# Performance work log

Hardware: AMD Instinct MI355X
Metric: run time of the kernel (lower is better)

The kernel has to match this reference:

```python
import jax, jax.numpy as jnp
import numpy as np

B, T, D = 2, 2048, 2048
H, HKV, DH = 16, 4, 128  # n_heads, n_kv_heads, d_head
EPS = 1e-6


def _rms_norm(t):
    # normalize over last dim, no learned weight (matches F.rms_norm default)
    return t * jax.lax.rsqrt(jnp.mean(t * t, axis=-1, keepdims=True) + EPS)


def _ortho_rope(t, cos, sin):
    # t: (b, h, t, d); unfold(-1,2,2) -> even/odd pairs
    x0 = t[..., 0::2]  # (b,h,t,d/2)
    x1 = t[..., 1::2]
    y0 = x0 * cos - x1 * sin
    y1 = x1 * cos + x0 * sin
    # NOTE: concatenated halves (NOT re-interleaved), faithful to source
    return jnp.concatenate((y0, y1), axis=-1)


def setup_inputs() -> dict:
    key = jax.random.key(0)
    ks = jax.random.split(key, 10)
    return {
        "x": jax.random.normal(ks[0], (B, T, D), jnp.float32),
        "pos_ids": jnp.broadcast_to(jnp.arange(T, dtype=jnp.int64), (B, T)),
        "cos": jax.random.normal(ks[1], (T, DH // 2), jnp.float32),
        "sin": jax.random.normal(ks[2], (T, DH // 2), jnp.float32),
        "v1": jax.random.normal(ks[3], (B, HKV, T, DH), jnp.float32),
        "Wq": jax.random.normal(ks[4], (H * DH, D), jnp.float32) * (D ** -0.5),
        "Wk": jax.random.normal(ks[5], (HKV * DH, D), jnp.float32) * (D ** -0.5),
        "Wv": jax.random.normal(ks[6], (HKV * DH, D), jnp.float32) * (D ** -0.5),
        "Wo": jax.random.normal(ks[7], (D, D), jnp.float32) * (D ** -0.5),
        "gate_w": jax.random.normal(ks[8], (H, H), jnp.float32) * 0.1,
        "v_lamb": jnp.float32(0.5),
    }


def reference(x, pos_ids, cos, sin, v1, Wq, Wk, Wv, Wo, gate_w, v_lamb):
    b, t, _ = x.shape
    # fused QKV projections (Linear, no bias: x @ W.T), split to heads
    q = (x @ Wq.T).reshape(b, t, H, DH).transpose(0, 2, 1, 3)    # (b,H,t,d)
    k = (x @ Wk.T).reshape(b, t, HKV, DH).transpose(0, 2, 1, 3)  # (b,Hkv,t,d)
    v = (x @ Wv.T).reshape(b, t, HKV, DH).transpose(0, 2, 1, 3)
    # value residual: lerp(v, v1, lamb) = v + lamb*(v1 - v)
    v = v + v_lamb * (v1 - v)
    # QK RMSNorm then ortho RoPE
    q = _ortho_rope(_rms_norm(q), cos, sin)
    k = _ortho_rope(_rms_norm(k), cos, sin)
    # kv_cache.upsert modeled as prefill: k,v unchanged, causal block mask
    g = H // HKV  # GQA group size
    k = jnp.repeat(k, g, axis=1)  # (b,H,t,d)
    vfull = jnp.repeat(v, g, axis=1)
    scale = DH ** -0.5
    scores = jnp.einsum('bhqd,bhkd->bhqk', q, k) * scale
    causal = jnp.tril(jnp.ones((t, t), dtype=bool))
    scores = jnp.where(causal, scores, jnp.finfo(scores.dtype).min)
    attn = jax.nn.softmax(scores, axis=-1)
    y = jnp.einsum('bhqk,bhkd->bhqd', attn, vfull)  # (b,H,t,d)
    # per-head sigmoid gate from first n_heads channels of x
    gates = jax.nn.sigmoid(x[..., :H] @ gate_w.T)   # (b,t,H)
    y = y * gates.transpose(0, 2, 1)[..., None]     # (b,H,t,1)
    y = y.transpose(0, 2, 1, 3).reshape(b, t, H * DH)
    out = y @ Wo.T
    return (out, v1)
```

## Files before the change

kernel.cpp:

```cpp
#include <hip/hip_runtime.h>

typedef __bf16 bf16;
typedef __attribute__((ext_vector_type(8))) __bf16 bf16x8;
typedef __attribute__((ext_vector_type(4))) __bf16 bf16x4;
typedef __attribute__((ext_vector_type(4))) float f32x4;
typedef __attribute__((ext_vector_type(4))) short short4v;

#define BB 2
#define TT 2048
#define DD 2048
#define HH 16
#define HKV 4
#define DHD 128
#define NQKV 3072

__device__ __forceinline__ void gl_lds16(const bf16* g, bf16* l) {
    __builtin_amdgcn_global_load_lds(
        (const __attribute__((address_space(1))) void*)g,
        (__attribute__((address_space(3))) void*)l, 16, 0, 0);
}

__global__ void cvt_fuse(const float* __restrict__ x, const float* __restrict__ Wq,
                         const float* __restrict__ Wk, const float* __restrict__ Wv,
                         const float* __restrict__ Wo, const float* __restrict__ gw,
                         bf16* __restrict__ xb, bf16* __restrict__ wqkvb,
                         bf16* __restrict__ wob, float* __restrict__ gates) {
    const int blk = blockIdx.x, tid = threadIdx.x;
    const float* src; bf16* dst; int i;
    const bool isx = blk < 4096;
    if (isx)              { src = x;  dst = xb;              i = blk * 256 + tid; }
    else if (blk < 6144)  { src = Wq; dst = wqkvb;           i = (blk - 4096) * 256 + tid; }
    else if (blk < 6656)  { src = Wk; dst = wqkvb + 4194304; i = (blk - 6144) * 256 + tid; }
    else if (blk < 7168)  { src = Wv; dst = wqkvb + 5242880; i = (blk - 6656) * 256 + tid; }
    else                  { src = Wo; dst = wob;             i = (blk - 7168) * 256 + tid; }
    float4 a = ((const float4*)src)[i * 2];
    float4 b = ((const float4*)src)[i * 2 + 1];
    bf16x8 v;
    v[0] = (bf16)a.x; v[1] = (bf16)a.y; v[2] = (bf16)a.z; v[3] = (bf16)a.w;
    v[4] = (bf16)b.x; v[5] = (bf16)b.y; v[6] = (bf16)b.z; v[7] = (bf16)b.w;
    *(bf16x8*)(dst + (size_t)i * 8) = v;

    if (isx) {
        __shared__ float xs16[16];
        __shared__ float gws[256];
        gws[tid] = gw[tid];
        if (tid < 2) {
            xs16[tid * 8 + 0] = a.x; xs16[tid * 8 + 1] = a.y;
            xs16[tid * 8 + 2] = a.z; xs16[tid * 8 + 3] = a.w;
            xs16[tid * 8 + 4] = b.x; xs16[tid * 8 + 5] = b.y;
            xs16[tid * 8 + 6] = b.z; xs16[tid * 8 + 7] = b.w;
        }
        __syncthreads();
        if (tid < 16) {
            float z = 0.f;
#pragma unroll
            for (int j = 0; j < 16; j++) z += xs16[j] * gws[tid * 16 + j];
            gates[blk * 16 + tid] = 1.f / (1.f + __expf(-z));
        }
    }
}

template <int MODE>
__global__ void gemm_bt(const bf16* __restrict__ A, const bf16* __restrict__ Bw,
                        int M, int N, int K,
                        float* __restrict__ Cout,
                        bf16* __restrict__ qb, bf16* __restrict__ kb,
                        bf16* __restrict__ vtb,
                        const float* __restrict__ v1,
                        const float* __restrict__ cosb,
                        const float* __restrict__ sinb,
                        const float* __restrict__ lamp) {
    constexpr int SMEM_ELE = (MODE == 1) ? 17920 : 16384;
    __shared__ bf16 smem[SMEM_ELE];
    bf16* As = smem;
    bf16* Bs = smem + 8192;
    const int tid = threadIdx.x;
    const int w = tid >> 6, lane = tid & 63;
    const int l15 = lane & 15, quad = lane >> 4;

    const int nwg = gridDim.x * gridDim.y;
    int wg = blockIdx.y * gridDim.x + blockIdx.x;
    int swz = (wg & 7) * (nwg >> 3) + (wg >> 3);
    const int bx = swz % gridDim.x, by = swz / gridDim.x;
    const int m0 = by * 128, n0 = bx * 128;
    const int wm = (w & 1) * 64, wn = (w >> 1) * 64;

    f32x4 acc[4][4] = {};
    const int lrow = lane >> 2;
    const int scol = ((lane & 3) ^ ((lane >> 3) & 3)) * 8;
    const int xs = (quad ^ ((l15 >> 1) & 3)) * 8;

    for (int k0 = 0; k0 < K; k0 += 64) {
#pragma unroll
        for (int i = 0; i < 4; i++) {
            int c = w * 4 + i;
            int kc2 = c >> 3, rc = c & 7;
            int row = rc * 16 + lrow;
            int kk = k0 + kc2 * 32 + scol;
            gl_lds16(A + (size_t)(m0 + row) * K + kk, As + c * 512);
            gl_lds16(Bw + (size_t)(n0 + row) * K + kk, Bs + c * 512);
        }
        __syncthreads();
#pragma unroll
        for (int kc2 = 0; kc2 < 2; kc2++) {
            bf16x8 af[4], bfr[4];
#pragma unroll
            for (int mi = 0; mi < 4; mi++)
                af[mi] = *(const bf16x8*)(As + kc2 * 4096 + ((wm >> 4) + mi) * 512 + l15 * 32 + xs);
#pragma unroll
            for (int ni = 0; ni < 4; ni++)
                bfr[ni] = *(const bf16x8*)(Bs + kc2 * 4096 + ((wn >> 4) + ni) * 512 + l15 * 32 + xs);
#pragma unroll
            for (int mi = 0; mi < 4; mi++)
#pragma unroll
                for (int ni = 0; ni < 4; ni++)
                    acc[mi][ni] = __builtin_amdgcn_mfma_f32_16x16x32_bf16(af[mi], bfr[ni], acc[mi][ni], 0, 0, 0);
        }
        __syncthreads();
    }

    if constexpr (MODE == 0) {
#pragma unroll
        for (int mi = 0; mi < 4; mi++)
#pragma unroll
            for (int ni = 0; ni < 4; ni++)
#pragma unroll
                for (int r = 0; r < 4; r++) {
                    int m = m0 + wm + mi * 16 + quad * 4 + r;
                    int n = n0 + wn + ni * 16 + l15;
                    Cout[(size_t)m * N + n] = acc[mi][ni][r];
                }
    } else {
        const int hid = n0 >> 7;
        const int b = m0 >> 11;
        const int t0 = m0 & (TT - 1);
        bf16* ep = smem;

        if (hid < 20) {
            float* ssum = (float*)(smem + 17408);
            float ssq[4][4];
#pragma unroll
            for (int mi = 0; mi < 4; mi++)
#pragma unroll
                for (int r = 0; r < 4; r++) {
                    float s = 0.f;
#pragma unroll
                    for (int ni = 0; ni < 4; ni++) {
                        float v = acc[mi][ni][r];
                        s += v * v;
                    }
                    s += __shfl_xor(s, 1);
                    s += __shfl_xor(s, 2);
                    s += __shfl_xor(s, 4);
                    s += __shfl_xor(s, 8);
                    ssq[mi][r] = s;
                }
            if (l15 == 0) {
#pragma unroll
                for (int mi = 0; mi < 4; mi++)
#pragma unroll
                    for (int r = 0; r < 4; r++)
                        ssum[(wn >> 6) * 128 + wm + mi * 16 + quad * 4 + r] = ssq[mi][r];
            }
            __syncthreads();
            const float QSCALE = 0.08838834764831845f * 1.4426950408889634f;
            float rn[4][4];
#pragma unroll
            for (int mi = 0; mi < 4; mi++)
#pragma unroll
                for (int r = 0; r < 4; r++) {
                    int row = wm + mi * 16 + quad * 4 + r;
                    float ss = ssum[row] + ssum[128 + row];
                    float rv = rsqrtf(ss * (1.f / 128.f) + 1e-6f);
                    if (hid < HH) rv *= QSCALE;
                    rn[mi][r] = rv;
                }
#pragma unroll
            for (int mi = 0; mi < 4; mi++)
#pragma unroll
                for (int ni = 0; ni < 4; ni++)
#pragma unroll
                    for (int r = 0; r < 4; r++) {
                        float sv = acc[mi][ni][r] * rn[mi][r];
                        float pv = __shfl_xor(sv, 1);
                        int nl = wn + ni * 16 + l15;
                        int j = nl >> 1;
                        int tl = wm + mi * 16 + quad * 4 + r;
                        float c = cosb[(size_t)(t0 + tl) * 64 + j];
                        float s = sinb[(size_t)(t0 + tl) * 64 + j];
                        float o = (nl & 1) ? (sv * c + pv * s) : (sv * c - pv * s);
                        int oc = (nl & 1) ? (64 + j) : j;
                        ep[tl * 136 + oc] = (bf16)o;
                    }
            __syncthreads();
            bf16* dst = (hid < HH)
                ? (qb + ((size_t)(b * HH + hid) * TT + t0) * DHD)
                : (kb + ((size_t)(b * HKV + (hid - HH)) * TT + t0) * DHD);
            int tl = tid >> 1, half = tid & 1;
#pragma unroll
            for (int c8 = 0; c8 < 8; c8++)
                *(bf16x8*)(dst + (size_t)tl * DHD + half * 64 + c8 * 8) =
                    *(const bf16x8*)(ep + tl * 136 + half * 64 + c8 * 8);
        } else {
            float lam = lamp[0];
            int vh = hid - 20;
            const float* v1b = v1 + ((size_t)(b * HKV + vh) * TT) * DHD;
#pragma unroll
            for (int mi = 0; mi < 4; mi++)
#pragma unroll
            for (int ni = 0; ni < 4; ni++)
#pragma unroll
                for (int r = 0; r < 4; r++) {
                    int d = wn + ni * 16 + l15;
                    int tl = wm + mi * 16 + quad * 4 + r;
                    float val = acc[mi][ni][r];
                    float vm = val + lam * (v1b[(size_t)(t0 + tl) * DHD + d] - val);
                    ep[d * 136 + tl] = (bf16)vm;
                }
            __syncthreads();
            bf16* dstv = vtb + ((size_t)(b * HKV + vh) * DHD) * TT + t0;
            int dd = tid >> 1, half = tid & 1;
#pragma unroll
            for (int c8 = 0; c8 < 8; c8++)
                *(bf16x8*)(dstv + (size_t)dd * TT + half * 64 + c8 * 8) =
                    *(const bf16x8*)(ep + dd * 136 + half * 64 + c8 * 8);
        }
    }
}

__global__ __launch_bounds__(256, 2) void fattn(const bf16* __restrict__ qbuf,
                                                const bf16* __restrict__ kbuf,
                                                const bf16* __restrict__ vt,
                                                const float* __restrict__ gates,
                                                bf16* __restrict__ yb,
                                                const float* __restrict__ v1f,
                                                float* __restrict__ vout) {
    __shared__ bf16 Ks[2][8192];
    __shared__ bf16 VTs[2][8192];

    const int bid = blockIdx.x;
    const int bh = bid & 31;
    const int gg = bid >> 5;
    const int g = gg & 7, qhalf = gg >> 3;
    const int h = bh & 15, b = bh >> 4;
    const int hk = h >> 2;
    const int tid = threadIdx.x, wq = tid >> 6, lane = tid & 63;
    const int l15 = lane & 15, quad = lane >> 4;

    {
        const float4* s4 = (const float4*)(v1f + (size_t)bid * 4096);
        float4* d4 = (float4*)(vout + (size_t)bid * 4096);
#pragma unroll
        for (int i = 0; i < 4; i++) d4[tid + i * 256] = s4[tid + i * 256];
    }

    const bf16* qbase = qbuf + ((size_t)(b * HH + h) * TT) * DHD;
    const bf16* kbase = kbuf + ((size_t)(b * HKV + hk) * TT) * DHD;
    const bf16* vtbase = vt + ((size_t)(b * HKV + hk) * DHD) * TT;

    const int Tq0 = qhalf ? (15 - g) : g;
    const int Tq1 = qhalf ? (16 + g) : (31 - g);
    const int ktmax_blk = Tq1;

    bf16x8 qf0[4], qf1[4];
#pragma unroll
    for (int kc = 0; kc < 4; kc++) {
        qf0[kc] = *(const bf16x8*)(qbase + (size_t)(Tq0 * 64 + wq * 16 + l15) * DHD + kc * 32 + quad * 8);
        qf1[kc] = *(const bf16x8*)(qbase + (size_t)(Tq1 * 64 + wq * 16 + l15) * DHD + kc * 32 + quad * 8);
    }

    bool dm[4][4];
#pragma unroll
    for (int ni = 0; ni < 4; ni++)
#pragma unroll
        for (int r = 0; r < 4; r++)
            dm[ni][r] = ((ni >> 1) * 32 + quad * 8 + (ni & 1) * 4 + r) > (wq * 16 + l15);

    const int srow = lane >> 2;
    const int gst = (((lane >> 5) & 1) << 1) | ((lane >> 3) & 1);
    const int scg = ((lane & 3) ^ gst) * 8;
    const int vrow = lane >> 3;
    const int vcg = ((lane & 7) ^ ((lane >> 3) & 7)) * 8;

    auto stage = [&](int kt, int buf) {
#pragma unroll
        for (int i = 0; i < 4; i++)
            gl_lds16(kbase + (size_t)(kt * 64 + wq * 16 + srow) * DHD + i * 32 + scg,
                     &Ks[buf][i * 2048 + wq * 512]);
#pragma unroll
        for (int i = 0; i < 4; i++)
            gl_lds16(vtbase + (size_t)(wq * 32 + i * 8 + vrow) * TT + kt * 64 + vcg,
                     &VTs[buf][wq * 2048 + i * 512]);
    };

    stage(0, 0);

    const int gk = (((l15 >> 2) & 1) << 1) | ((l15 >> 1) & 1);

    f32x4 O0[8] = {}, O1[8] = {};
    float m0 = -INFINITY, l0 = 0.f, m1 = -INFINITY, l1 = 0.f;

    union PW { bf16x4 h[2]; bf16x8 v; };

    for (int kt = 0; kt <= ktmax_blk; kt++) {
        int cur = kt & 1;
        __syncthreads();
        if (kt < ktmax_blk) stage(kt + 1, cur ^ 1);

        const bool a0 = (kt <= Tq0);

        f32x4 s0[4], s1[4];
        __builtin_amdgcn_s_setprio(1);
#pragma unroll
        for (int ni = 0; ni < 4; ni++) {
            int rr = (ni >> 1) * 32 + (l15 >> 2) * 8 + (ni & 1) * 4 + (l15 & 3);
            bf16x8 kfl[4];
#pragma unroll
            for (int kc = 0; kc < 4; kc++)
                kfl[kc] = *(const bf16x8*)(&Ks[cur][kc * 2048 + rr * 32 + ((quad ^ gk) * 8)]);
            f32x4 z1 = {};
#pragma unroll
            for (int kc = 0; kc < 4; kc++)
                z1 = __builtin_amdgcn_mfma_f32_16x16x32_bf16(kfl[kc], qf1[kc], z1, 0, 0, 0);
            s1[ni] = z1;
            if (a0) {
                f32x4 z0 = {};
#pragma unroll
                for (int kc = 0; kc < 4; kc++)
                    z0 = __builtin_amdgcn_mfma_f32_16x16x32_bf16(kfl[kc], qf0[kc], z0, 0, 0, 0);
                s0[ni] = z0;
            }
        }
        __builtin_amdgcn_s_setprio(0);

        PW pw0[2], pw1[2];
        {
            if (kt == Tq1) {
#pragma unroll
                for (int ni = 0; ni < 4; ni++)
#pragma unroll
                    for (int r = 0; r < 4; r++)
                        if (dm[ni][r]) s1[ni][r] = -INFINITY;
            }
            float mx = s1[0][0];
#pragma unroll
            for (int ni = 0; ni < 4; ni++)
#pragma unroll
                for (int r = 0; r < 4; r++) mx = fmaxf(mx, s1[ni][r]);
            mx = fmaxf(mx, __shfl_xor(mx, 16));
            mx = fmaxf(mx, __shfl_xor(mx, 32));
            float mold = m1;
            bool noresc = __all(mx <= mold + 8.f);
            float mnew = noresc ? mold : fmaxf(mold, mx);
            float rs = 0.f;
#pragma unroll
            for (int ni = 0; ni < 4; ni++) {
                bf16x4 hv;
#pragma unroll
                for (int r = 0; r < 4; r++) {
                    float pe = __builtin_amdgcn_exp2f(s1[ni][r] - mnew);
                    hv[r] = (bf16)pe;
                    rs += pe;
                }
                pw1[ni >> 1].h[ni & 1] = hv;
            }
            rs += __shfl_xor(rs, 16);
            rs += __shfl_xor(rs, 32);
            if (!noresc) {
                float al = __builtin_amdgcn_exp2f(mold - mnew);
                l1 *= al;
#pragma unroll
                for (int dn = 0; dn < 8; dn++)
#pragma unroll
                    for (int r = 0; r < 4; r++) O1[dn][r] *= al;
                m1 = mnew;
            }
            l1 += rs;
        }
        if (a0) {
            if (kt == Tq0) {
#pragma unroll
                for (int ni = 0; ni < 4; ni++)
#pragma unroll
                    for (int r = 0; r < 4; r++)
                        if (dm[ni][r]) s0[ni][r] = -INFINITY;
            }
            float mx = s0[0][0];
#pragma unroll
            for (int ni = 0; ni < 4; ni++)
#pragma unroll
                for (int r = 0; r < 4; r++) mx = fmaxf(mx, s0[ni][r]);
            mx = fmaxf(mx, __shfl_xor(mx, 16));
            mx = fmaxf(mx, __shfl_xor(mx, 32));
            float mold = m0;
            bool noresc = __all(mx <= mold + 8.f);
            float mnew = noresc ? mold : fmaxf(mold, mx);
            float rs = 0.f;
#pragma unroll
            for (int ni = 0; ni < 4; ni++) {
                bf16x4 hv;
#pragma unroll
                for (int r = 0; r < 4; r++) {
                    float pe = __builtin_amdgcn_exp2f(s0[ni][r] - mnew);
                    hv[r] = (bf16)pe;
                    rs += pe;
                }
                pw0[ni >> 1].h[ni & 1] = hv;
            }
            rs += __shfl_xor(rs, 16);
            rs += __shfl_xor(rs, 32);
            if (!noresc) {
                float al = __builtin_amdgcn_exp2f(mold - mnew);
                l0 *= al;
#pragma unroll
                for (int dn = 0; dn < 8; dn++)
#pragma unroll
                    for (int r = 0; r < 4; r++) O0[dn][r] *= al;
                m0 = mnew;
            }
            l0 += rs;
        }

        __builtin_amdgcn_s_setprio(1);
#pragma unroll
        for (int ni2 = 0; ni2 < 2; ni2++) {
            bf16x8 vfl[8];
#pragma unroll
            for (int dn = 0; dn < 8; dn++)
                vfl[dn] = *(const bf16x8*)(&VTs[cur][(dn * 16 + l15) * 64 +
                                                    (((ni2 * 4 + quad) ^ (l15 & 7)) * 8)]);
#pragma unroll
            for (int dn = 0; dn < 8; dn++)
                O1[dn] = __builtin_amdgcn_mfma_f32_16x16x32_bf16(vfl[dn], pw1[ni2].v, O1[dn], 0, 0, 0);
            if (a0) {
#pragma unroll
                for (int dn = 0; dn < 8; dn++)
                    O0[dn] = __builtin_amdgcn_mfma_f32_16x16x32_bf16(vfl[dn], pw0[ni2].v, O0[dn], 0, 0, 0);
            }
        }
        __builtin_amdgcn_s_setprio(0);
    }

    auto epi = [&](const f32x4* Oc, float lsum, int qt) {
        int qg = qt * 64 + wq * 16 + l15;
        float gi = gates[((size_t)b * TT + qg) * HH + h] / lsum;
#pragma unroll
        for (int dn = 0; dn < 8; dn++) {
            bf16x4 o;
#pragma unroll
            for (int r = 0; r < 4; r++) o[r] = (bf16)(Oc[dn][r] * gi);
            *(bf16x4*)(yb + ((size_t)(b * TT + qg) * HH + h) * DHD + dn * 16 + quad * 4) = o;
        }
    };
    epi(O0, l0, Tq0);
    epi(O1, l1, Tq1);
}

extern "C" void kernel_launch(void* const* d_in, const int* in_sizes, int n_in,
                              void* d_out, int out_size, void* d_ws, size_t ws_size,
                              hipStream_t stream) {
    const float* x    = (const float*)d_in[0];
    const float* cosb = (const float*)d_in[2];
    const float* sinb = (const float*)d_in[3];
    const float* v1   = (const float*)d_in[4];
    const float* Wq   = (const float*)d_in[5];
    const float* Wk   = (const float*)d_in[6];
    const float* Wv   = (const float*)d_in[7];
    const float* Wo   = (const float*)d_in[8];
    const float* gw   = (const float*)d_in[9];
    const float* lam  = (const float*)d_in[10];
    float* out = (float*)d_out;

    char* ws = (char*)d_ws;
    bf16* xb     = (bf16*)(ws);
    bf16* wqkvb  = (bf16*)(ws + 16777216);
    bf16* wob    = (bf16*)(ws + 29360128);
    bf16* qb     = (bf16*)(ws + 79691776);
    bf16* kb     = (bf16*)(ws + 96468992);
    bf16* vtb    = (bf16*)(ws + 100663296);
    float* gts   = (float*)(ws + 104857600);
    bf16* yb     = xb;

    cvt_fuse<<<9216, 256, 0, stream>>>(x, Wq, Wk, Wv, Wo, gw, xb, wqkvb, wob, gts);

    gemm_bt<1><<<dim3(24, 32), 256, 0, stream>>>(xb, wqkvb, 4096, NQKV, 2048,
                                                 nullptr, qb, kb, vtb, v1,
                                                 cosb, sinb, lam);
    fattn<<<512, 256, 0, stream>>>(qb, kb, vtb, gts, yb, v1, out + 8388608);
    gemm_bt<0><<<dim3(16, 32), 256, 0, stream>>>(yb, wob, 4096, 2048, 2048,
                                                 out, nullptr, nullptr, nullptr,
                                                 nullptr, nullptr, nullptr, nullptr);
}
```

Before: 287.5 us.

## Replace QKV GEMM with 256x256-tile, 4-stage pipelined kernel with fused epilogue

```diff
diff --git a/kernel.cpp b/kernel.cpp
--- a/kernel.cpp
+++ b/kernel.cpp
@@ -60,18 +60,196 @@
     }
 }
 
+__global__ __launch_bounds__(512, 2)
+void gemm_qkv256(const bf16* __restrict__ A, const bf16* __restrict__ Bw,
+                 bf16* __restrict__ qb, bf16* __restrict__ kb,
+                 bf16* __restrict__ vtb,
+                 const float* __restrict__ v1,
+                 const float* __restrict__ cosb,
+                 const float* __restrict__ sinb,
+                 const float* __restrict__ lamp) {
+    __shared__ bf16 smem[65536];
+    bf16* As = smem;
+    bf16* Bs = smem + 32768;
+    const int tid = threadIdx.x;
+    const int w = tid >> 6, lane = tid & 63;
+    const int l15 = lane & 15, quad = lane >> 4;
+    const int wr = w >> 2, wc = w & 3;
+
+    const int nwg = gridDim.x * gridDim.y;
+    int wg = blockIdx.y * gridDim.x + blockIdx.x;
+    int swz = (wg & 7) * (nwg >> 3) + (wg >> 3);
+    const int bx = swz % gridDim.x, by = swz / gridDim.x;
+    const int m0 = by * 256, n0 = bx * 256;
+
+    const int srow = lane >> 2;
+    const int sck = ((lane & 3) ^ ((lane >> 3) & 3)) * 8;
+    const int xs = (quad ^ ((l15 >> 1) & 3)) * 8;
+
+    auto stage = [&](int j) {
+        int jc = j > 63 ? 63 : j;
+        int slot = j & 3;
+        size_t kk = (size_t)(jc << 5) + sck;
+#pragma unroll
+        for (int i = 0; i < 2; i++) {
+            int row = w * 32 + i * 16 + srow;
+            gl_lds16(A + (size_t)(m0 + row) * 2048 + kk,
+                     As + slot * 8192 + w * 1024 + i * 512);
+            gl_lds16(Bw + (size_t)(n0 + row) * 2048 + kk,
+                     Bs + slot * 8192 + w * 1024 + i * 512);
+        }
+    };
+
+    f32x4 acc[8][4] = {};
+    bf16x8 af[8], bfv[4];
+
+    auto rdfrags = [&](int j) {
+        int slot = j & 3;
+        const bf16* Ab = As + slot * 8192 + (wr * 128) * 32;
+        const bf16* Bb = Bs + slot * 8192 + (wc * 64) * 32;
+#pragma unroll
+        for (int mi = 0; mi < 8; mi++)
+            af[mi] = *(const bf16x8*)(Ab + (mi * 16 + l15) * 32 + xs);
+#pragma unroll
+        for (int ni = 0; ni < 4; ni++)
+            bfv[ni] = *(const bf16x8*)(Bb + (ni * 16 + l15) * 32 + xs);
+    };
+
+    stage(0); stage(1); stage(2);
+    asm volatile("s_waitcnt vmcnt(8)" ::: "memory");
+    __builtin_amdgcn_s_barrier();
+    asm volatile("" ::: "memory");
+    rdfrags(0);
+
+    for (int j = 0; j < 64; j++) {
+        asm volatile("s_waitcnt vmcnt(4)" ::: "memory");
+        __builtin_amdgcn_s_barrier();
+        asm volatile("" ::: "memory");
+        asm volatile("s_waitcnt lgkmcnt(0)" ::: "memory");
+        __builtin_amdgcn_sched_barrier(0);
+        stage(j + 3);
+        __builtin_amdgcn_s_setprio(1);
+#pragma unroll
+        for (int mi = 0; mi < 8; mi++)
+#pragma unroll
+            for (int ni = 0; ni < 4; ni++)
+                acc[mi][ni] = __builtin_amdgcn_mfma_f32_16x16x32_bf16(af[mi], bfv[ni], acc[mi][ni], 0, 0, 0);
+        __builtin_amdgcn_s_setprio(0);
+        rdfrags(j + 1);
+    }
+    __syncthreads();
+
+    const int hp2 = n0 >> 7;
+    const int b = m0 >> 11;
+    const int t0 = m0 & (TT - 1);
+    bf16* ep = smem;
+    float* ssum = (float*)((char*)smem + 69632);
+
+    const float QSCALE = 0.08838834764831845f * 1.4426950408889634f;
+    float lam = (hp2 >= 20) ? lamp[0] : 0.f;
+
+#pragma unroll
+    for (int rh = 0; rh < 2; rh++) {
+        if (hp2 < 20) {
+            if (wr == rh) {
+#pragma unroll
+                for (int mi = 0; mi < 8; mi++)
+#pragma unroll
+                    for (int r = 0; r < 4; r++) {
+                        float s = 0.f;
+#pragma unroll
+                        for (int ni = 0; ni < 4; ni++) {
+                            float vv = acc[mi][ni][r];
+                            s += vv * vv;
+                        }
+                        s += __shfl_xor(s, 1);
+                        s += __shfl_xor(s, 2);
+                        s += __shfl_xor(s, 4);
+                        s += __shfl_xor(s, 8);
+                        if (l15 == 0) ssum[wc * 128 + mi * 16 + quad * 4 + r] = s;
+                    }
+            }
+            __syncthreads();
+            if (wr == rh) {
+#pragma unroll
+                for (int mi = 0; mi < 8; mi++) {
+                    float rn[4];
+#pragma unroll
+                    for (int r = 0; r < 4; r++) {
+                        int row = mi * 16 + quad * 4 + r;
+                        float ss = ssum[(wc & ~1) * 128 + row] + ssum[((wc & ~1) | 1) * 128 + row];
+                        float rv = rsqrtf(ss * (1.f / 128.f) + 1e-6f);
+                        if (hp2 < HH) rv *= QSCALE;
+                        rn[r] = rv;
+                    }
+#pragma unroll
+                    for (int ni = 0; ni < 4; ni++)
+#pragma unroll
+                        for (int r = 0; r < 4; r++) {
+                            float sv = acc[mi][ni][r] * rn[r];
+                            float pv = __shfl_xor(sv, 1);
+                            int nl = (wc & 1) * 64 + ni * 16 + l15;
+                            int jj = nl >> 1;
+                            int tl = mi * 16 + quad * 4 + r;
+                            float c = cosb[(size_t)(t0 + rh * 128 + tl) * 64 + jj];
+                            float s = sinb[(size_t)(t0 + rh * 128 + tl) * 64 + jj];
+                            float o = (nl & 1) ? (sv * c + pv * s) : (sv * c - pv * s);
+                            int oc = (nl & 1) ? (64 + jj) : jj;
+                            ep[(wc >> 1) * 17408 + tl * 136 + oc] = (bf16)o;
+                        }
+                }
+            }
+            __syncthreads();
+            int tl = tid >> 2, sg = tid & 3;
+#pragma unroll
+            for (int hd = 0; hd < 2; hd++) {
+                int hg = hp2 + hd;
+                bf16* dst = (hp2 < HH)
+                    ? (qb + ((size_t)(b * HH + hg) * TT + t0 + rh * 128) * DHD)
+                    : (kb + ((size_t)(b * HKV + (hg - HH)) * TT + t0 + rh * 128) * DHD);
+#pragma unroll
+                for (int c8 = 0; c8 < 4; c8++)
+                    *(bf16x8*)(dst + (size_t)tl * DHD + sg * 8 + c8 * 32) =
+                        *(const bf16x8*)(ep + hd * 17408 + tl * 136 + sg * 8 + c8 * 32);
+            }
+            __syncthreads();
+        } else {
+            if (wr == rh) {
+#pragma unroll
+                for (int mi = 0; mi < 8; mi++)
+#pragma unroll
+                    for (int ni = 0; ni < 4; ni++)
+#pragma unroll
+                        for (int r = 0; r < 4; r++) {
+                            int d = (wc & 1) * 64 + ni * 16 + l15;
+                            int tl = mi * 16 + quad * 4 + r;
+                            int vh = hp2 - 20 + (wc >> 1);
+                            float val = acc[mi][ni][r];
+                            float vm = val + lam * (v1[((size_t)(b * HKV + vh) * TT + t0 + rh * 128 + tl) * DHD + d] - val);
+                            ep[(wc >> 1) * 17408 + d * 136 + tl] = (bf16)vm;
+                        }
+            }
+            __syncthreads();
+            int dd = tid >> 2, sg = tid & 3;
+#pragma unroll
+            for (int hd = 0; hd < 2; hd++) {
+                int vh = hp2 - 20 + hd;
+                bf16* dstv = vtb + ((size_t)(b * HKV + vh) * DHD + dd) * TT + t0 + rh * 128;
+#pragma unroll
+                for (int c8 = 0; c8 < 4; c8++)
+                    *(bf16x8*)(dstv + sg * 8 + c8 * 32) =
+                        *(const bf16x8*)(ep + hd * 17408 + dd * 136 + sg * 8 + c8 * 32);
+            }
+            __syncthreads();
+        }
+    }
+}
+
 template <int MODE>
 __global__ void gemm_bt(const bf16* __restrict__ A, const bf16* __restrict__ Bw,
                         int M, int N, int K,
-                        float* __restrict__ Cout,
-                        bf16* __restrict__ qb, bf16* __restrict__ kb,
-                        bf16* __restrict__ vtb,
-                        const float* __restrict__ v1,
-                        const float* __restrict__ cosb,
-                        const float* __restrict__ sinb,
-                        const float* __restrict__ lamp) {
-    constexpr int SMEM_ELE = (MODE == 1) ? 17920 : 16384;
-    __shared__ bf16 smem[SMEM_ELE];
+                        float* __restrict__ Cout) {
+    __shared__ bf16 smem[16384];
     bf16* As = smem;
     bf16* Bs = smem + 8192;
     const int tid = threadIdx.x;
@@ -119,113 +297,16 @@
         __syncthreads();
     }
 
-    if constexpr (MODE == 0) {
-#pragma unroll
-        for (int mi = 0; mi < 4; mi++)
-#pragma unroll
-            for (int ni = 0; ni < 4; ni++)
-#pragma unroll
-                for (int r = 0; r < 4; r++) {
-                    int m = m0 + wm + mi * 16 + quad * 4 + r;
-                    int n = n0 + wn + ni * 16 + l15;
-                    Cout[(size_t)m * N + n] = acc[mi][ni][r];
-                }
-    } else {
-        const int hid = n0 >> 7;
-        const int b = m0 >> 11;
-        const int t0 = m0 & (TT - 1);
-        bf16* ep = smem;
-
-        if (hid < 20) {
-            float* ssum = (float*)(smem + 17408);
-            float ssq[4][4];
-#pragma unroll
-            for (int mi = 0; mi < 4; mi++)
-#pragma unroll
-                for (int r = 0; r < 4; r++) {
-                    float s = 0.f;
-#pragma unroll
-                    for (int ni = 0; ni < 4; ni++) {
-                        float v = acc[mi][ni][r];
-                        s += v * v;
-                    }
-                    s += __shfl_xor(s, 1);
-                    s += __shfl_xor(s, 2);
-                    s += __shfl_xor(s, 4);
-                    s += __shfl_xor(s, 8);
-                    ssq[mi][r] = s;
-                }
-            if (l15 == 0) {
-#pragma unroll
-                for (int mi = 0; mi < 4; mi++)
-#pragma unroll
-                    for (int r = 0; r < 4; r++)
-                        ssum[(wn >> 6) * 128 + wm + mi * 16 + quad * 4 + r] = ssq[mi][r];
-            }
-            __syncthreads();
-            const float QSCALE = 0.08838834764831845f * 1.4426950408889634f;
-            float rn[4][4];
-#pragma unroll
-            for (int mi = 0; mi < 4; mi++)
-#pragma unroll
-                for (int r = 0; r < 4; r++) {
-                    int row = wm + mi * 16 + quad * 4 + r;
-                    float ss = ssum[row] + ssum[128 + row];
-                    float rv = rsqrtf(ss * (1.f / 128.f) + 1e-6f);
-                    if (hid < HH) rv *= QSCALE;
-                    rn[mi][r] = rv;
-                }
-#pragma unroll
-            for (int mi = 0; mi < 4; mi++)
-#pragma unroll
-                for (int ni = 0; ni < 4; ni++)
-#pragma unroll
-                    for (int r = 0; r < 4; r++) {
-                        float sv = acc[mi][ni][r] * rn[mi][r];
-                        float pv = __shfl_xor(sv, 1);
-                        int nl = wn + ni * 16 + l15;
-                        int j = nl >> 1;
-                        int tl = wm + mi * 16 + quad * 4 + r;
-                        float c = cosb[(size_t)(t0 + tl) * 64 + j];
-                        float s = sinb[(size_t)(t0 + tl) * 64 + j];
-                        float o = (nl & 1) ? (sv * c + pv * s) : (sv * c - pv * s);
-                        int oc = (nl & 1) ? (64 + j) : j;
-                        ep[tl * 136 + oc] = (bf16)o;
-                    }
-            __syncthreads();
-            bf16* dst = (hid < HH)
-                ? (qb + ((size_t)(b * HH + hid) * TT + t0) * DHD)
-                : (kb + ((size_t)(b * HKV + (hid - HH)) * TT + t0) * DHD);
-            int tl = tid >> 1, half = tid & 1;
-#pragma unroll
-            for (int c8 = 0; c8 < 8; c8++)
-                *(bf16x8*)(dst + (size_t)tl * DHD + half * 64 + c8 * 8) =
-                    *(const bf16x8*)(ep + tl * 136 + half * 64 + c8 * 8);
-        } else {
-            float lam = lamp[0];
-            int vh = hid - 20;
-            const float* v1b = v1 + ((size_t)(b * HKV + vh) * TT) * DHD;
-#pragma unroll
-            for (int mi = 0; mi < 4; mi++)
-#pragma unroll
-            for (int ni = 0; ni < 4; ni++)
-#pragma unroll
-                for (int r = 0; r < 4; r++) {
-                    int d = wn + ni * 16 + l15;
-                    int tl = wm + mi * 16 + quad * 4 + r;
-                    float val = acc[mi][ni][r];
-                    float vm = val + lam * (v1b[(size_t)(t0 + tl) * DHD + d] - val);
-                    ep[d * 136 + tl] = (bf16)vm;
-                }
-            __syncthreads();
-            bf16* dstv = vtb + ((size_t)(b * HKV + vh) * DHD) * TT + t0;
-            int dd = tid >> 1, half = tid & 1;
-#pragma unroll
-            for (int c8 = 0; c8 < 8; c8++)
-                *(bf16x8*)(dstv + (size_t)dd * TT + half * 64 + c8 * 8) =
-                    *(const bf16x8*)(ep + dd * 136 + half * 64 + c8 * 8);
-        }
-    }
+#pragma unroll
+    for (int mi = 0; mi < 4; mi++)
+#pragma unroll
+        for (int ni = 0; ni < 4; ni++)
+#pragma unroll
+            for (int r = 0; r < 4; r++) {
+                int m = m0 + wm + mi * 16 + quad * 4 + r;
+                int n = n0 + wn + ni * 16 + l15;
+                Cout[(size_t)m * N + n] = acc[mi][ni][r];
+            }
 }
 
 __global__ __launch_bounds__(256, 2) void fattn(const bf16* __restrict__ qbuf,
@@ -483,11 +564,8 @@
 
     cvt_fuse<<<9216, 256, 0, stream>>>(x, Wq, Wk, Wv, Wo, gw, xb, wqkvb, wob, gts);
 
-    gemm_bt<1><<<dim3(24, 32), 256, 0, stream>>>(xb, wqkvb, 4096, NQKV, 2048,
-                                                 nullptr, qb, kb, vtb, v1,
-                                                 cosb, sinb, lam);
+    gemm_qkv256<<<dim3(12, 16), 512, 0, stream>>>(xb, wqkvb, qb, kb, vtb, v1,
+                                                  cosb, sinb, lam);
     fattn<<<512, 256, 0, stream>>>(qb, kb, vtb, gts, yb, v1, out + 8388608);
-    gemm_bt<0><<<dim3(16, 32), 256, 0, stream>>>(yb, wob, 4096, 2048, 2048,
-                                                 out, nullptr, nullptr, nullptr,
-                                                 nullptr, nullptr, nullptr, nullptr);
+    gemm_bt<0><<<dim3(16, 32), 256, 0, stream>>>(yb, wob, 4096, 2048, 2048, out);
 }
```

After: 300.4 us. 4.5% more time.
